# Kernel optimization log

Measured on AMD Instinct MI355X. Metric: run time of the kernel, lower is better.

## Reference

```python
import jax, jax.numpy as jnp
import numpy as np

N = 50000       # nodes
E = 800000      # edges
NUM_IN, NUM_HID, NUM_OUT = 128, 32, 40
K = 2           # ARMA stacks (both convs)
T = 2           # ARMA layers per conv (shared weights)


def setup_inputs() -> dict:
    key = jax.random.key(0)
    ks = jax.random.split(key, 12)
    def glorot(k, shape, fan_in):
        return jax.random.normal(k, shape, jnp.float32) / np.sqrt(fan_in)
    return {
        "x": jax.random.normal(ks[0], (N, NUM_IN), jnp.float32),
        "edge_index": jax.random.randint(ks[1], (2, E), 0, N, dtype=jnp.int32),
        "w1_init": glorot(ks[2], (K, NUM_IN, NUM_HID), NUM_IN),
        "w1_deep": glorot(ks[3], (K, NUM_HID, NUM_HID), NUM_HID),
        "w1_root": glorot(ks[4], (K, NUM_IN, NUM_HID), NUM_IN),
        "b1": jnp.zeros((K, NUM_HID), jnp.float32),
        "w2_init": glorot(ks[5], (K, NUM_HID, NUM_OUT), NUM_HID),
        "w2_deep": glorot(ks[6], (K, NUM_OUT, NUM_OUT), NUM_OUT),
        "w2_root": glorot(ks[7], (K, NUM_HID, NUM_OUT), NUM_HID),
        "b2": jnp.zeros((K, NUM_OUT), jnp.float32),
    }


def _gcn_norm(row, col, n, dtype):
    # symmetric norm without self loops (PyG ARMAConv default)
    deg = jax.ops.segment_sum(jnp.ones(row.shape[0], dtype), col, num_segments=n)
    dinv = jnp.where(deg > 0, jax.lax.rsqrt(jnp.maximum(deg, 1e-12)), 0.0).astype(dtype)
    return dinv[row] * dinv[col]  # [E]


def _arma_conv(x, row, col, ew, w_init, w_deep, w_root, b, use_act):
    # x: [N, F_in] -> out: [N, F_out]; K stacks, T shared-weight layers
    n = x.shape[0]
    root = jnp.einsum('nf,kfh->nkh', x, w_root)   # [N, K, F_out] (shared root weight)
    out = jnp.einsum('nf,kfh->nkh', x, w_init)
    for t in range(T):
        if t > 0:
            out = jnp.einsum('nkh,khg->nkg', out, w_deep)
        msg = out[row] * ew[:, None, None]         # gather at source, [E, K, F_out]
        out = jax.ops.segment_sum(msg, col, num_segments=n)  # scatter-add at target
        out = out + root + b[None, :, :]
        if use_act:
            out = jax.nn.relu(out)
    return out.mean(axis=1)  # mean over stacks


def reference(x, edge_index, w1_init, w1_deep, w1_root, b1,
              w2_init, w2_deep, w2_root, b2):
    row, col = edge_index[0], edge_index[1]
    ew = _gcn_norm(row, col, x.shape[0], x.dtype)
    h1 = _arma_conv(x, row, col, ew, w1_init, w1_deep, w1_root, b1, use_act=True)
    h = jax.nn.relu(h1)
    h2 = _arma_conv(h, row, col, ew, w2_init, w2_deep, w2_root, b2, use_act=False)
    return jax.nn.log_softmax(h2, axis=1)
```

## Files before the change

### kernel.cpp

```cpp
#include <hip/hip_runtime.h>
#include <math.h>


typedef unsigned short ushort_t;
typedef __attribute__((ext_vector_type(8))) short  short8v;
typedef __attribute__((ext_vector_type(4))) float  float4v;

__device__ inline ushort_t f2bf(float v) {
    unsigned u = __float_as_uint(v);
    u += 0x7FFFu + ((u >> 16) & 1u);
    return (ushort_t)(u >> 16);
}
__device__ inline float2 unpack2(unsigned p) {
    return make_float2(__uint_as_float(p << 16), __uint_as_float(p & 0xFFFF0000u));
}

__global__ void k_hist(const int* __restrict__ col, int* __restrict__ deg, int e) {
    int i = blockIdx.x * blockDim.x + threadIdx.x;
    if (i < e) atomicAdd(&deg[col[i]], 1);
}

__global__ void k_dinv(const int* __restrict__ deg, float* __restrict__ dinv, int n) {
    int i = blockIdx.x * blockDim.x + threadIdx.x;
    if (i < n) {
        int d = deg[i];
        dinv[i] = d > 0 ? rsqrtf((float)d) : 0.0f;
    }
}

__global__ void k_scan1(const int* __restrict__ deg, int* __restrict__ start,
                        int* __restrict__ bsum, int n) {
    __shared__ int s[256];
    int t = threadIdx.x, idx = blockIdx.x * 256 + t;
    int v = (idx < n) ? deg[idx] : 0;
    s[t] = v; __syncthreads();
    for (int o = 1; o < 256; o <<= 1) {
        int x = (t >= o) ? s[t - o] : 0;
        __syncthreads(); s[t] += x; __syncthreads();
    }
    if (idx <= n) start[idx] = s[t] - v;
    if (t == 255) bsum[blockIdx.x] = s[255];
}

__global__ void k_scan2(const int* __restrict__ bsum, int* __restrict__ bscan) {
    __shared__ int s[256];
    int t = threadIdx.x;
    int v = bsum[t]; s[t] = v; __syncthreads();
    for (int o = 1; o < 256; o <<= 1) {
        int x = (t >= o) ? s[t - o] : 0;
        __syncthreads(); s[t] += x; __syncthreads();
    }
    bscan[t] = s[t] - v;
}

__global__ void k_scan3(int* __restrict__ start, int* __restrict__ cursor,
                        const int* __restrict__ bscan, int n) {
    int idx = blockIdx.x * 256 + threadIdx.x;
    if (idx <= n) {
        int v = start[idx] + bscan[idx >> 8];
        start[idx] = v;
        if (idx < n) cursor[idx] = v;
    }
}

__global__ void k_sort(const int* __restrict__ row, const int* __restrict__ col,
                       const float* __restrict__ dinv, int* __restrict__ cursor,
                       int2* __restrict__ sedge, int e) {
    int i = blockIdx.x * blockDim.x + threadIdx.x;
    if (i < e) {
        int r = row[i], c = col[i];
        int pos = atomicAdd(&cursor[c], 1);
        sedge[pos] = make_int2(r, __float_as_int(dinv[r] * dinv[c]));
    }
}

__global__ void k_wprep(const float* __restrict__ wi, const float* __restrict__ wr,
                        ushort_t* __restrict__ Wt, int K, int F, int H) {
    int idx = blockIdx.x * blockDim.x + threadIdx.x;
    int tot = 2 * K * H * F;
    if (idx >= tot) return;
    int f = idx % F, colx = idx / F;
    int KH = K * H;
    const float* src = (colx < KH) ? wi : wr;
    int c = (colx < KH) ? colx : colx - KH;
    int k = c / H, h = c % H;
    Wt[idx] = f2bf(src[((long)k * F + f) * H + h]);
}

__global__ void k_wprep_diag(const float* __restrict__ w, ushort_t* __restrict__ Wt,
                             int K, int F, int FPAD) {
    int idx = blockIdx.x * blockDim.x + threadIdx.x;
    int tot = K * F * FPAD;
    if (idx >= tot) return;
    int kin = idx % FPAD, colx = idx / FPAD;
    int k = colx / F, h = colx % F;
    float v = 0.0f;
    if (kin < K * F) {
        int kp = kin / F, f = kin % F;
        if (kp == k) v = w[((long)k * F + f) * F + h];
    }
    Wt[idx] = f2bf(v);
}

template<int FIN, int FPAD, int NCOLT, int KF0, bool SPLIT>
__global__ void k_mfma_gemm(const float* __restrict__ X,
                            const ushort_t* __restrict__ Wt,
                            ushort_t* __restrict__ out0,
                            float* __restrict__ root,
                            int n) {
    constexpr int KSTEPS = FPAD / 32;
    int wid  = (blockIdx.x * blockDim.x + threadIdx.x) >> 6;
    int lane = threadIdx.x & 63;
    int m0 = wid * 16;
    if (m0 >= n) return;
    int r = lane & 15, g = lane >> 4;
    float4v acc[NCOLT];
#pragma unroll
    for (int c = 0; c < NCOLT; ++c) acc[c] = (float4v){0.f, 0.f, 0.f, 0.f};
#pragma unroll
    for (int ks = 0; ks < KSTEPS; ++ks) {
        int kb = ks * 32 + g * 8;
        const float* xr = X + (long)(m0 + r) * FIN + kb;
        float4 x0 = *(const float4*)xr;
        float4 x1 = *(const float4*)(xr + 4);
        short8v af;
        af[0] = (short)f2bf(x0.x); af[1] = (short)f2bf(x0.y);
        af[2] = (short)f2bf(x0.z); af[3] = (short)f2bf(x0.w);
        af[4] = (short)f2bf(x1.x); af[5] = (short)f2bf(x1.y);
        af[6] = (short)f2bf(x1.z); af[7] = (short)f2bf(x1.w);
#pragma unroll
        for (int c = 0; c < NCOLT; ++c) {
            short8v bf = *(const short8v*)&Wt[(long)(c * 16 + r) * FPAD + kb];
            acc[c] = __builtin_amdgcn_mfma_f32_16x16x32_bf16(af, bf, acc[c], 0, 0, 0);
        }
    }
#pragma unroll
    for (int c = 0; c < NCOLT; ++c) {
        int colx = c * 16 + r;
#pragma unroll
        for (int i = 0; i < 4; ++i) {
            long node = m0 + g * 4 + i;
            if (!SPLIT || colx < KF0)
                out0[node * KF0 + colx] = f2bf(acc[c][i]);
            else
                root[node * KF0 + (colx - KF0)] = acc[c][i];
        }
    }
}

template<int MODE>
__global__ void k_gather64(const ushort_t* __restrict__ A, const int2* __restrict__ sedge,
                           const int* __restrict__ start, const float* __restrict__ root,
                           const float* __restrict__ bias, float* __restrict__ out,
                           int npairs) {
    const unsigned* A32 = (const unsigned*)A;
    int gid = blockIdx.x * blockDim.x + threadIdx.x;
    int q = gid >> 5, sub = gid & 31;
    if (q >= npairs) return;
    int na = 2 * q, nb = 2 * q + 1;
    float2 bi   = *(const float2*)&bias[2 * sub];
    float2 acca = *(const float2*)&root[(long)na * 64 + 2 * sub];
    float2 accb = *(const float2*)&root[(long)nb * 64 + 2 * sub];
    acca.x += bi.x; acca.y += bi.y;
    accb.x += bi.x; accb.y += bi.y;
    int ea = start[na], e1a = start[na + 1];
    int eb = start[nb], e1b = start[nb + 1];
    while (ea < e1a && eb < e1b) {
        int2 pa = sedge[ea]; int2 pb = sedge[eb];
        float2 va = unpack2(A32[(long)pa.x * 32 + sub]);
        float2 vb = unpack2(A32[(long)pb.x * 32 + sub]);
        float wa = __int_as_float(pa.y), wb = __int_as_float(pb.y);
        acca.x = fmaf(va.x, wa, acca.x); acca.y = fmaf(va.y, wa, acca.y);
        accb.x = fmaf(vb.x, wb, accb.x); accb.y = fmaf(vb.y, wb, accb.y);
        ++ea; ++eb;
    }
    for (; ea < e1a; ++ea) {
        int2 p = sedge[ea];
        float2 v = unpack2(A32[(long)p.x * 32 + sub]);
        float w = __int_as_float(p.y);
        acca.x = fmaf(v.x, w, acca.x); acca.y = fmaf(v.y, w, acca.y);
    }
    for (; eb < e1b; ++eb) {
        int2 p = sedge[eb];
        float2 v = unpack2(A32[(long)p.x * 32 + sub]);
        float w = __int_as_float(p.y);
        accb.x = fmaf(v.x, w, accb.x); accb.y = fmaf(v.y, w, accb.y);
    }
    if (MODE == 1) {
        *(float2*)&out[(long)na * 64 + 2 * sub] = make_float2(fmaxf(acca.x, 0.f), fmaxf(acca.y, 0.f));
        *(float2*)&out[(long)nb * 64 + 2 * sub] = make_float2(fmaxf(accb.x, 0.f), fmaxf(accb.y, 0.f));
    } else {
        float2 va = make_float2(fmaxf(acca.x, 0.f), fmaxf(acca.y, 0.f));
        float2 vb = make_float2(fmaxf(accb.x, 0.f), fmaxf(accb.y, 0.f));
        float2 oa = make_float2(__shfl_xor(va.x, 16), __shfl_xor(va.y, 16));
        float2 ob = make_float2(__shfl_xor(vb.x, 16), __shfl_xor(vb.y, 16));
        if (sub < 16) {
            *(float2*)&out[(long)na * 32 + 2 * sub] =
                make_float2(0.5f * (va.x + oa.x), 0.5f * (va.y + oa.y));
            *(float2*)&out[(long)nb * 32 + 2 * sub] =
                make_float2(0.5f * (vb.x + ob.x), 0.5f * (vb.y + ob.y));
        }
    }
}

__global__ void k_gather80(const ushort_t* __restrict__ A, const int2* __restrict__ sedge,
                           const int* __restrict__ start, const float* __restrict__ root,
                           const float* __restrict__ bias, float* __restrict__ out,
                           int npairs) {
    const unsigned* A32 = (const unsigned*)A;
    int gid = blockIdx.x * blockDim.x + threadIdx.x;
    int q = gid / 40, f2 = gid % 40;
    if (q >= npairs) return;
    int na = 2 * q, nb = 2 * q + 1;
    float2 bi   = *(const float2*)&bias[2 * f2];
    float2 acca = *(const float2*)&root[(long)na * 80 + 2 * f2];
    float2 accb = *(const float2*)&root[(long)nb * 80 + 2 * f2];
    acca.x += bi.x; acca.y += bi.y;
    accb.x += bi.x; accb.y += bi.y;
    int ea = start[na], e1a = start[na + 1];
    int eb = start[nb], e1b = start[nb + 1];
    while (ea < e1a && eb < e1b) {
        int2 pa = sedge[ea]; int2 pb = sedge[eb];
        float2 va = unpack2(A32[(long)pa.x * 40 + f2]);
        float2 vb = unpack2(A32[(long)pb.x * 40 + f2]);
        float wa = __int_as_float(pa.y), wb = __int_as_float(pb.y);
        acca.x = fmaf(va.x, wa, acca.x); acca.y = fmaf(va.y, wa, acca.y);
        accb.x = fmaf(vb.x, wb, accb.x); accb.y = fmaf(vb.y, wb, accb.y);
        ++ea; ++eb;
    }
    for (; ea < e1a; ++ea) {
        int2 p = sedge[ea];
        float2 v = unpack2(A32[(long)p.x * 40 + f2]);
        float w = __int_as_float(p.y);
        acca.x = fmaf(v.x, w, acca.x); acca.y = fmaf(v.y, w, acca.y);
    }
    for (; eb < e1b; ++eb) {
        int2 p = sedge[eb];
        float2 v = unpack2(A32[(long)p.x * 40 + f2]);
        float w = __int_as_float(p.y);
        accb.x = fmaf(v.x, w, accb.x); accb.y = fmaf(v.y, w, accb.y);
    }
    *(float2*)&out[(long)na * 80 + 2 * f2] = acca;
    *(float2*)&out[(long)nb * 80 + 2 * f2] = accb;
}

__global__ void k_logsoftmax(const float* __restrict__ B, float* __restrict__ out, int n) {
    int gid  = blockIdx.x * blockDim.x + threadIdx.x;
    int wave = gid >> 6;
    int lane = gid & 63;
    if (wave >= n) return;
    float v = -INFINITY;
    if (lane < 40)
        v = 0.5f * (B[(long)wave * 80 + lane] + B[(long)wave * 80 + 40 + lane]);
    float m = v;
#pragma unroll
    for (int o = 32; o; o >>= 1) m = fmaxf(m, __shfl_xor(m, o));
    float ex = (lane < 40) ? expf(v - m) : 0.0f;
    float s = ex;
#pragma unroll
    for (int o = 32; o; o >>= 1) s += __shfl_xor(s, o);
    if (lane < 40) out[(long)wave * 40 + lane] = v - m - logf(s);
}

extern "C" void kernel_launch(void* const* d_in, const int* in_sizes, int n_in,
                              void* d_out, int out_size, void* d_ws, size_t ws_size,
                              hipStream_t stream) {
    const float* x       = (const float*)d_in[0];
    const int*   eidx    = (const int*)d_in[1];
    const float* w1_init = (const float*)d_in[2];
    const float* w1_deep = (const float*)d_in[3];
    const float* w1_root = (const float*)d_in[4];
    const float* b1      = (const float*)d_in[5];
    const float* w2_init = (const float*)d_in[6];
    const float* w2_deep = (const float*)d_in[7];
    const float* w2_root = (const float*)d_in[8];
    const float* b2      = (const float*)d_in[9];
    float* out = (float*)d_out;

    const int N = in_sizes[0] / 128;
    const int E = in_sizes[1] / 2;
    const int* row = eidx;
    const int* col = eidx + E;

    int2*     sedge  = (int2*)d_ws;
    int*      start  = (int*)(sedge + E);
    ushort_t* A      = (ushort_t*)(start + N + 4);
    float*    B      = (float*)(A + (long)N * 80);
    float*    root   = B + (long)N * 80;
    ushort_t* Wt1    = (ushort_t*)(root + (long)N * 80);
    ushort_t* Wt2    = Wt1 + 128 * 128;
    ushort_t* Wtd1   = Wt2 + 160 * 32;
    ushort_t* Wtd2   = Wtd1 + 64 * 64;
    int*      deg_i  = (int*)(Wtd2 + 80 * 96);
    int*      cursor = deg_i + N;
    int*      bsum   = cursor + N;
    int*      bscan  = bsum + 256;
    float*    dinv   = (float*)(bscan + 256);
    float*    h      = B;

    const int BS = 256;
    auto cdiv = [](long a, long b) { return (int)((a + b - 1) / b); };
    const int NP = N / 2;
    const int MT = cdiv(N, 16);

    hipMemsetAsync(deg_i, 0, (size_t)N * 4, stream);
    k_hist<<<cdiv(E, BS), BS, 0, stream>>>(col, deg_i, E);
    k_dinv<<<cdiv(N, BS), BS, 0, stream>>>(deg_i, dinv, N);
    k_scan1<<<256, 256, 0, stream>>>(deg_i, start, bsum, N);
    k_scan2<<<1, 256, 0, stream>>>(bsum, bscan);
    k_scan3<<<256, 256, 0, stream>>>(start, cursor, bscan, N);
    k_sort<<<cdiv(E, BS), BS, 0, stream>>>(row, col, dinv, cursor, sedge, E);
    k_wprep<<<cdiv(2 * 2 * 32 * 128, BS), BS, 0, stream>>>(w1_init, w1_root, Wt1, 2, 128, 32);
    k_wprep<<<cdiv(2 * 2 * 40 * 32, BS), BS, 0, stream>>>(w2_init, w2_root, Wt2, 2, 32, 40);
    k_wprep_diag<<<cdiv(64 * 64, BS), BS, 0, stream>>>(w1_deep, Wtd1, 2, 32, 64);
    k_wprep_diag<<<cdiv(80 * 96, BS), BS, 0, stream>>>(w2_deep, Wtd2, 2, 40, 96);

    k_mfma_gemm<128, 128, 8, 64, true><<<cdiv(MT, 4), 256, 0, stream>>>(x, Wt1, A, root, N);
    k_gather64<1><<<cdiv((long)NP * 32, BS), BS, 0, stream>>>(A, sedge, start, root, b1, B, NP);
    k_mfma_gemm<64, 64, 4, 64, false><<<cdiv(MT, 4), 256, 0, stream>>>(B, Wtd1, A, nullptr, N);
    k_gather64<2><<<cdiv((long)NP * 32, BS), BS, 0, stream>>>(A, sedge, start, root, b1, h, NP);

    k_mfma_gemm<32, 32, 10, 80, true><<<cdiv(MT, 4), 256, 0, stream>>>(h, Wt2, A, root, N);
    k_gather80<<<cdiv((long)NP * 40, 320), 320, 0, stream>>>(A, sedge, start, root, b2, B, NP);
    k_mfma_gemm<80, 96, 5, 80, false><<<cdiv(MT, 4), 256, 0, stream>>>(B, Wtd2, A, nullptr, N);
    k_gather80<<<cdiv((long)NP * 40, 320), 320, 0, stream>>>(A, sedge, start, root, b2, B, NP);

    k_logsoftmax<<<cdiv((long)N * 64, BS), BS, 0, stream>>>(B, out, N);
}
```

Baseline: 441.0 us.

## Split gather features into per-stack halves for cache-resident neighbor reads

```diff
diff --git a/kernel.cpp b/kernel.cpp
--- a/kernel.cpp
+++ b/kernel.cpp
@@ -5,14 +5,19 @@
 typedef unsigned short ushort_t;
 typedef __attribute__((ext_vector_type(8))) short  short8v;
 typedef __attribute__((ext_vector_type(4))) float  float4v;
+typedef __attribute__((ext_vector_type(2))) float  f32x2;
+typedef __attribute__((ext_vector_type(2))) int    i32x2;
 
 __device__ inline ushort_t f2bf(float v) {
     unsigned u = __float_as_uint(v);
     u += 0x7FFFu + ((u >> 16) & 1u);
     return (ushort_t)(u >> 16);
 }
-__device__ inline float2 unpack2(unsigned p) {
-    return make_float2(__uint_as_float(p << 16), __uint_as_float(p & 0xFFFF0000u));
+__device__ inline f32x2 unpack2(unsigned p) {
+    f32x2 r;
+    r[0] = __uint_as_float(p << 16);
+    r[1] = __uint_as_float(p & 0xFFFF0000u);
+    return r;
 }
 
 __global__ void k_hist(const int* __restrict__ col, int* __restrict__ deg, int e) {
@@ -102,7 +107,7 @@
     Wt[idx] = f2bf(v);
 }
 
-template<int FIN, int FPAD, int NCOLT, int KF0, bool SPLIT>
+template<int FIN, int FPAD, int NCOLT, int KF0, int HALF, bool SPLIT>
 __global__ void k_mfma_gemm(const float* __restrict__ X,
                             const ushort_t* __restrict__ Wt,
                             ushort_t* __restrict__ out0,
@@ -140,108 +145,77 @@
 #pragma unroll
         for (int i = 0; i < 4; ++i) {
             long node = m0 + g * 4 + i;
-            if (!SPLIT || colx < KF0)
-                out0[node * KF0 + colx] = f2bf(acc[c][i]);
-            else
+            if (!SPLIT || colx < KF0) {
+                int hf = colx / HALF, f = colx - hf * HALF;
+                out0[((long)hf * n + node) * HALF + f] = f2bf(acc[c][i]);
+            } else {
                 root[node * KF0 + (colx - KF0)] = acc[c][i];
+            }
         }
     }
 }
 
-template<int MODE>
-__global__ void k_gather64(const ushort_t* __restrict__ A, const int2* __restrict__ sedge,
-                           const int* __restrict__ start, const float* __restrict__ root,
-                           const float* __restrict__ bias, float* __restrict__ out,
-                           int npairs) {
-    const unsigned* A32 = (const unsigned*)A;
+template<int HALF, int MODE>
+__global__ void k_gatherH(const ushort_t* __restrict__ Ah, const int2* __restrict__ sedge,
+                          const int* __restrict__ start, const float* __restrict__ root,
+                          const float* __restrict__ bias, float* __restrict__ out,
+                          int rootStride, int outStride, int npairs) {
+    constexpr int LPN = HALF / 2;
+    const unsigned* A32 = (const unsigned*)Ah;
     int gid = blockIdx.x * blockDim.x + threadIdx.x;
-    int q = gid >> 5, sub = gid & 31;
+    int q = gid / LPN, sub = gid % LPN;
     if (q >= npairs) return;
     int na = 2 * q, nb = 2 * q + 1;
-    float2 bi   = *(const float2*)&bias[2 * sub];
-    float2 acca = *(const float2*)&root[(long)na * 64 + 2 * sub];
-    float2 accb = *(const float2*)&root[(long)nb * 64 + 2 * sub];
-    acca.x += bi.x; acca.y += bi.y;
-    accb.x += bi.x; accb.y += bi.y;
+    f32x2 bi   = *(const f32x2*)&bias[2 * sub];
+    f32x2 acca = __builtin_nontemporal_load((const f32x2*)&root[(long)na * rootStride + 2 * sub]);
+    f32x2 accb = __builtin_nontemporal_load((const f32x2*)&root[(long)nb * rootStride + 2 * sub]);
+    acca += bi; accb += bi;
     int ea = start[na], e1a = start[na + 1];
     int eb = start[nb], e1b = start[nb + 1];
     while (ea < e1a && eb < e1b) {
-        int2 pa = sedge[ea]; int2 pb = sedge[eb];
-        float2 va = unpack2(A32[(long)pa.x * 32 + sub]);
-        float2 vb = unpack2(A32[(long)pb.x * 32 + sub]);
-        float wa = __int_as_float(pa.y), wb = __int_as_float(pb.y);
-        acca.x = fmaf(va.x, wa, acca.x); acca.y = fmaf(va.y, wa, acca.y);
-        accb.x = fmaf(vb.x, wb, accb.x); accb.y = fmaf(vb.y, wb, accb.y);
+        i32x2 pa = __builtin_nontemporal_load((const i32x2*)(sedge + ea));
+        i32x2 pb = __builtin_nontemporal_load((const i32x2*)(sedge + eb));
+        f32x2 va = unpack2(A32[(long)pa[0] * LPN + sub]);
+        f32x2 vb = unpack2(A32[(long)pb[0] * LPN + sub]);
+        float wa = __int_as_float(pa[1]), wb = __int_as_float(pb[1]);
+        acca[0] = fmaf(va[0], wa, acca[0]); acca[1] = fmaf(va[1], wa, acca[1]);
+        accb[0] = fmaf(vb[0], wb, accb[0]); accb[1] = fmaf(vb[1], wb, accb[1]);
         ++ea; ++eb;
     }
     for (; ea < e1a; ++ea) {
-        int2 p = sedge[ea];
-        float2 v = unpack2(A32[(long)p.x * 32 + sub]);
-        float w = __int_as_float(p.y);
-        acca.x = fmaf(v.x, w, acca.x); acca.y = fmaf(v.y, w, acca.y);
+        i32x2 p = __builtin_nontemporal_load((const i32x2*)(sedge + ea));
+        f32x2 v = unpack2(A32[(long)p[0] * LPN + sub]);
+        float w = __int_as_float(p[1]);
+        acca[0] = fmaf(v[0], w, acca[0]); acca[1] = fmaf(v[1], w, acca[1]);
     }
     for (; eb < e1b; ++eb) {
-        int2 p = sedge[eb];
-        float2 v = unpack2(A32[(long)p.x * 32 + sub]);
-        float w = __int_as_float(p.y);
-        accb.x = fmaf(v.x, w, accb.x); accb.y = fmaf(v.y, w, accb.y);
-    }
-    if (MODE == 1) {
-        *(float2*)&out[(long)na * 64 + 2 * sub] = make_float2(fmaxf(acca.x, 0.f), fmaxf(acca.y, 0.f));
-        *(float2*)&out[(long)nb * 64 + 2 * sub] = make_float2(fmaxf(accb.x, 0.f), fmaxf(accb.y, 0.f));
+        i32x2 p = __builtin_nontemporal_load((const i32x2*)(sedge + eb));
+        f32x2 v = unpack2(A32[(long)p[0] * LPN + sub]);
+        float w = __int_as_float(p[1]);
+        accb[0] = fmaf(v[0], w, accb[0]); accb[1] = fmaf(v[1], w, accb[1]);
+    }
+    float* oa = out + (long)na * outStride + 2 * sub;
+    float* ob = out + (long)nb * outStride + 2 * sub;
+    if (MODE == 0) {
+        __builtin_nontemporal_store(acca, (f32x2*)oa);
+        __builtin_nontemporal_store(accb, (f32x2*)ob);
+    } else if (MODE == 1) {
+        f32x2 ra, rb;
+        ra[0] = fmaxf(acca[0], 0.f); ra[1] = fmaxf(acca[1], 0.f);
+        rb[0] = fmaxf(accb[0], 0.f); rb[1] = fmaxf(accb[1], 0.f);
+        __builtin_nontemporal_store(ra, (f32x2*)oa);
+        __builtin_nontemporal_store(rb, (f32x2*)ob);
     } else {
-        float2 va = make_float2(fmaxf(acca.x, 0.f), fmaxf(acca.y, 0.f));
-        float2 vb = make_float2(fmaxf(accb.x, 0.f), fmaxf(accb.y, 0.f));
-        float2 oa = make_float2(__shfl_xor(va.x, 16), __shfl_xor(va.y, 16));
-        float2 ob = make_float2(__shfl_xor(vb.x, 16), __shfl_xor(vb.y, 16));
-        if (sub < 16) {
-            *(float2*)&out[(long)na * 32 + 2 * sub] =
-                make_float2(0.5f * (va.x + oa.x), 0.5f * (va.y + oa.y));
-            *(float2*)&out[(long)nb * 32 + 2 * sub] =
-                make_float2(0.5f * (vb.x + ob.x), 0.5f * (vb.y + ob.y));
-        }
-    }
-}
-
-__global__ void k_gather80(const ushort_t* __restrict__ A, const int2* __restrict__ sedge,
-                           const int* __restrict__ start, const float* __restrict__ root,
-                           const float* __restrict__ bias, float* __restrict__ out,
-                           int npairs) {
-    const unsigned* A32 = (const unsigned*)A;
-    int gid = blockIdx.x * blockDim.x + threadIdx.x;
-    int q = gid / 40, f2 = gid % 40;
-    if (q >= npairs) return;
-    int na = 2 * q, nb = 2 * q + 1;
-    float2 bi   = *(const float2*)&bias[2 * f2];
-    float2 acca = *(const float2*)&root[(long)na * 80 + 2 * f2];
-    float2 accb = *(const float2*)&root[(long)nb * 80 + 2 * f2];
-    acca.x += bi.x; acca.y += bi.y;
-    accb.x += bi.x; accb.y += bi.y;
-    int ea = start[na], e1a = start[na + 1];
-    int eb = start[nb], e1b = start[nb + 1];
-    while (ea < e1a && eb < e1b) {
-        int2 pa = sedge[ea]; int2 pb = sedge[eb];
-        float2 va = unpack2(A32[(long)pa.x * 40 + f2]);
-        float2 vb = unpack2(A32[(long)pb.x * 40 + f2]);
-        float wa = __int_as_float(pa.y), wb = __int_as_float(pb.y);
-        acca.x = fmaf(va.x, wa, acca.x); acca.y = fmaf(va.y, wa, acca.y);
-        accb.x = fmaf(vb.x, wb, accb.x); accb.y = fmaf(vb.y, wb, accb.y);
-        ++ea; ++eb;
-    }
-    for (; ea < e1a; ++ea) {
-        int2 p = sedge[ea];
-        float2 v = unpack2(A32[(long)p.x * 40 + f2]);
-        float w = __int_as_float(p.y);
-        acca.x = fmaf(v.x, w, acca.x); acca.y = fmaf(v.y, w, acca.y);
-    }
-    for (; eb < e1b; ++eb) {
-        int2 p = sedge[eb];
-        float2 v = unpack2(A32[(long)p.x * 40 + f2]);
-        float w = __int_as_float(p.y);
-        accb.x = fmaf(v.x, w, accb.x); accb.y = fmaf(v.y, w, accb.y);
-    }
-    *(float2*)&out[(long)na * 80 + 2 * f2] = acca;
-    *(float2*)&out[(long)nb * 80 + 2 * f2] = accb;
+        f32x2 pa = *(const f32x2*)oa;
+        f32x2 pb = *(const f32x2*)ob;
+        f32x2 ra, rb;
+        ra[0] = 0.5f * (pa[0] + fmaxf(acca[0], 0.f));
+        ra[1] = 0.5f * (pa[1] + fmaxf(acca[1], 0.f));
+        rb[0] = 0.5f * (pb[0] + fmaxf(accb[0], 0.f));
+        rb[1] = 0.5f * (pb[1] + fmaxf(accb[1], 0.f));
+        __builtin_nontemporal_store(ra, (f32x2*)oa);
+        __builtin_nontemporal_store(rb, (f32x2*)ob);
+    }
 }
 
 __global__ void k_logsoftmax(const float* __restrict__ B, float* __restrict__ out, int n) {
@@ -315,15 +289,26 @@
     k_wprep_diag<<<cdiv(64 * 64, BS), BS, 0, stream>>>(w1_deep, Wtd1, 2, 32, 64);
     k_wprep_diag<<<cdiv(80 * 96, BS), BS, 0, stream>>>(w2_deep, Wtd2, 2, 40, 96);
 
-    k_mfma_gemm<128, 128, 8, 64, true><<<cdiv(MT, 4), 256, 0, stream>>>(x, Wt1, A, root, N);
-    k_gather64<1><<<cdiv((long)NP * 32, BS), BS, 0, stream>>>(A, sedge, start, root, b1, B, NP);
-    k_mfma_gemm<64, 64, 4, 64, false><<<cdiv(MT, 4), 256, 0, stream>>>(B, Wtd1, A, nullptr, N);
-    k_gather64<2><<<cdiv((long)NP * 32, BS), BS, 0, stream>>>(A, sedge, start, root, b1, h, NP);
-
-    k_mfma_gemm<32, 32, 10, 80, true><<<cdiv(MT, 4), 256, 0, stream>>>(h, Wt2, A, root, N);
-    k_gather80<<<cdiv((long)NP * 40, 320), 320, 0, stream>>>(A, sedge, start, root, b2, B, NP);
-    k_mfma_gemm<80, 96, 5, 80, false><<<cdiv(MT, 4), 256, 0, stream>>>(B, Wtd2, A, nullptr, N);
-    k_gather80<<<cdiv((long)NP * 40, 320), 320, 0, stream>>>(A, sedge, start, root, b2, B, NP);
+    ushort_t* Alo64 = A;
+    ushort_t* Ahi64 = A + (long)N * 32;
+    ushort_t* Alo80 = A;
+    ushort_t* Ahi80 = A + (long)N * 40;
+    const int G64 = cdiv((long)NP * 16, BS);
+    const int G80 = cdiv((long)NP * 20, 320);
+
+    k_mfma_gemm<128, 128, 8, 64, 32, true><<<cdiv(MT, 4), 256, 0, stream>>>(x, Wt1, A, root, N);
+    k_gatherH<32, 1><<<G64, BS, 0, stream>>>(Alo64, sedge, start, root,      b1,      B,      64, 64, NP);
+    k_gatherH<32, 1><<<G64, BS, 0, stream>>>(Ahi64, sedge, start, root + 32, b1 + 32, B + 32, 64, 64, NP);
+    k_mfma_gemm<64, 64, 4, 64, 32, false><<<cdiv(MT, 4), 256, 0, stream>>>(B, Wtd1, A, nullptr, N);
+    k_gatherH<32, 1><<<G64, BS, 0, stream>>>(Alo64, sedge, start, root,      b1,      h,      64, 32, NP);
+    k_gatherH<32, 3><<<G64, BS, 0, stream>>>(Ahi64, sedge, start, root + 32, b1 + 32, h,      64, 32, NP);
+
+    k_mfma_gemm<32, 32, 10, 80, 40, true><<<cdiv(MT, 4), 256, 0, stream>>>(h, Wt2, A, root, N);
+    k_gatherH<40, 0><<<G80, 320, 0, stream>>>(Alo80, sedge, start, root,      b2,      B,      80, 80, NP);
+    k_gatherH<40, 0><<<G80, 320, 0, stream>>>(Ahi80, sedge, start, root + 40, b2 + 40, B + 40, 80, 80, NP);
+    k_mfma_gemm<80, 96, 5, 80, 40, false><<<cdiv(MT, 4), 256, 0, stream>>>(B, Wtd2, A, nullptr, N);
+    k_gatherH<40, 0><<<G80, 320, 0, stream>>>(Alo80, sedge, start, root,      b2,      B,      80, 80, NP);
+    k_gatherH<40, 0><<<G80, 320, 0, stream>>>(Ahi80, sedge, start, root + 40, b2 + 40, B + 40, 80, 80, NP);
 
     k_logsoftmax<<<cdiv((long)N * 64, BS), BS, 0, stream>>>(B, out, N);
 }
```

New measurement: 603.9 us. 1.37x slower.
